# Performance work log

Hardware: AMD Instinct MI355X
Metric: run time of the kernel (lower is better)

Reference implementation:

```python
import jax, jax.numpy as jnp
import numpy as np

EPS = 1e-5

def spmm(rows, cols, vals, x, n_out):
    # COO sparse [n_out, n_in] @ x [n_in, d] -> [n_out, d]
    return jax.ops.segment_sum(vals[:, None] * x[cols], rows, num_segments=n_out)

def layernorm(x, g, b):
    mu = jnp.mean(x, axis=-1, keepdims=True)
    var = jnp.var(x, axis=-1, keepdims=True)
    return (x - mu) * jax.lax.rsqrt(var + EPS) * g + b

def setup_inputs() -> dict:
    key = jax.random.key(0)
    ks = jax.random.split(key, 32)
    N, D = 100000, 512
    N0, N1, N2 = 131072, 32768, 8192
    E_s0, E_s1 = 262144, 65536
    E_f0, E_f1 = 1048576, 262144
    s = 1.0 / np.sqrt(D)
    inp = {
        'x': jax.random.normal(ks[0], (N, D), jnp.float32),
        'hist0': jax.random.normal(ks[1], (N, D), jnp.float32),
        'hist1': jax.random.normal(ks[2], (N, D), jnp.float32),
        'w0': jax.random.normal(ks[3], (D, D), jnp.float32) * s,
        'b0': jax.random.normal(ks[4], (D,), jnp.float32) * s,
        'g0': jnp.ones((D,), jnp.float32),
        'beta0': jnp.zeros((D,), jnp.float32),
        'w1': jax.random.normal(ks[5], (D, D), jnp.float32) * s,
        'b1': jax.random.normal(ks[6], (D,), jnp.float32) * s,
        'sadj0_vals': jax.random.uniform(ks[7], (E_s0,), jnp.float32),
        'sadj1_vals': jax.random.uniform(ks[8], (E_s1,), jnp.float32),
        'fadj0_vals': jax.random.uniform(ks[9], (E_f0,), jnp.float32),
        'fadj1_vals': jax.random.uniform(ks[10], (E_f1,), jnp.float32),
        'sid0': jax.random.randint(ks[11], (N0,), 0, N),
        'sid1': jax.random.randint(ks[12], (N1,), 0, N),
        'sid2': jax.random.randint(ks[13], (N2,), 0, N),
        'fid0': jax.random.randint(ks[14], (N0,), 0, N),
        'fid1': jax.random.randint(ks[15], (N1,), 0, N),
        'sadj0_rows': jax.random.randint(ks[16], (E_s0,), 0, N1),
        'sadj0_cols': jax.random.randint(ks[17], (E_s0,), 0, N0),
        'sadj1_rows': jax.random.randint(ks[18], (E_s1,), 0, N2),
        'sadj1_cols': jax.random.randint(ks[19], (E_s1,), 0, N1),
        'fadj0_rows': jax.random.randint(ks[20], (E_f0,), 0, N1),
        'fadj0_cols': jax.random.randint(ks[21], (E_f0,), 0, N0),
        'fadj1_rows': jax.random.randint(ks[22], (E_f1,), 0, N2),
        'fadj1_cols': jax.random.randint(ks[23], (E_f1,), 0, N1),
    }
    return inp

def reference(x, hist0, hist1, w0, b0, g0, beta0, w1, b1,
              sadj0_vals, sadj1_vals, fadj0_vals, fadj1_vals,
              sid0, sid1, sid2, fid0, fid1,
              sadj0_rows, sadj0_cols, sadj1_rows, sadj1_cols,
              fadj0_rows, fadj0_cols, fadj1_rows, fadj1_cols):
    N1 = sid1.shape[0]
    N2 = sid2.shape[0]
    sg = jax.lax.stop_gradient
    # layer 0
    h = x[sid0]                                   # [N0, D]
    h = h - sg(hist0[sid0])                        # variance-reduction correction
    full = sg(spmm(fadj0_rows, fadj0_cols, fadj0_vals, hist0[fid0], N1))
    h = spmm(sadj0_rows, sadj0_cols, sadj0_vals, h, N1) + full  # [N1, D]
    h = h @ w0.T + b0
    h = jax.nn.relu(layernorm(h, g0, beta0))
    # layer 1 (last: no norm/relu)
    h = h - sg(hist1[sid1])
    full = sg(spmm(fadj1_rows, fadj1_cols, fadj1_vals, hist1[fid1], N2))
    h = spmm(sadj1_rows, sadj1_cols, sadj1_vals, h, N2) + full  # [N2, D]
    h = h @ w1.T + b1
    return jax.nn.log_softmax(h, axis=-1)
```

## Files before the change

kernel.cpp:

```cpp
#include <hip/hip_runtime.h>

#define D 512
#define NTAB 100000

typedef __bf16 bf16x8 __attribute__((ext_vector_type(8)));
typedef float f32x4 __attribute__((ext_vector_type(4)));
typedef float f32x2 __attribute__((ext_vector_type(2)));

__device__ __forceinline__ unsigned f2bf(float f){
  union { float f; unsigned u; } v; v.f = f;
  unsigned r = v.u + 0x7fffu + ((v.u >> 16) & 1u);
  return r >> 16;
}
__device__ __forceinline__ float bf2f(unsigned h){
  union { unsigned u; float f; } v; v.u = h << 16; return v.f;
}
__device__ __forceinline__ uint2 enc_fp8x8(f32x4 v0, f32x4 v1){
  int lo = __builtin_amdgcn_cvt_pk_fp8_f32(v0[0], v0[1], 0, false);
  lo     = __builtin_amdgcn_cvt_pk_fp8_f32(v0[2], v0[3], lo, true);
  int hi = __builtin_amdgcn_cvt_pk_fp8_f32(v1[0], v1[1], 0, false);
  hi     = __builtin_amdgcn_cvt_pk_fp8_f32(v1[2], v1[3], hi, true);
  return make_uint2((unsigned)lo, (unsigned)hi);
}

#define PER8 (NTAB*D/8)

#define MA_NS   6400
#define MA_GRID (MA_NS*5 + 512)

__global__ __launch_bounds__(256) void k_megaA(
    const int* __restrict__ s0r, int nS0,
    const int* __restrict__ f0r, int nF0, int* __restrict__ cnt0,
    const int* __restrict__ s1r, int nS1, int* __restrict__ cnt_s1,
    const int* __restrict__ f1r, int nF1, int* __restrict__ cnt_f1,
    const float* __restrict__ x, const float* __restrict__ hist0,
    unsigned char* __restrict__ TD,
    const float* __restrict__ w0, const float* __restrict__ w1,
    unsigned short* __restrict__ w0b, unsigned short* __restrict__ w1b)
{
  int b = blockIdx.x, t = threadIdx.x;
  if (b < MA_NS*5){
    int sb = b / 5, r = b % 5;
    if (r == 0){
      int i = sb*256 + t;
      if (i < nS0){ atomicAdd(&cnt0[s0r[i]], 1); return; }
      i -= nS0;
      if (i < nF0){ atomicAdd(&cnt0[f0r[i]], 1); return; }
      i -= nF0;
      if (i < nS1){ atomicAdd(&cnt_s1[s1r[i]], 1); return; }
      i -= nS1;
      atomicAdd(&cnt_f1[f1r[i]], 1);
      return;
    }
    {
      int ci = (sb*4 + (r-1))*256 + t;
      if (ci >= PER8) return;
      const f32x4* px = (const f32x4*)(x     + (size_t)ci*8);
      const f32x4* ph = (const f32x4*)(hist0 + (size_t)ci*8);
      f32x4 x0 = __builtin_nontemporal_load(px);
      f32x4 x1 = __builtin_nontemporal_load(px+1);
      f32x4 h0 = __builtin_nontemporal_load(ph);
      f32x4 h1 = __builtin_nontemporal_load(ph+1);
      *(uint2*)(TD + (size_t)ci*8)                    = enc_fp8x8(x0 - h0, x1 - h1);
      *(uint2*)(TD + (size_t)NTAB*D + (size_t)ci*8)   = enc_fp8x8(h0, h1);
      return;
    }
  } else {
    int i = (b - MA_NS*5)*256 + t;
    const float* src = (i < 65536) ? w0 : w1;
    unsigned short* dst = (i < 65536) ? w0b : w1b;
    int ii = (i < 65536) ? i : i - 65536;
    f32x4 v = *(const f32x4*)(src + (size_t)ii*4);
    ushort4 o;
    o.x = (unsigned short)f2bf(v[0]); o.y = (unsigned short)f2bf(v[1]);
    o.z = (unsigned short)f2bf(v[2]); o.w = (unsigned short)f2bf(v[3]);
    *(ushort4*)(dst + (size_t)ii*4) = o;
  }
}

__global__ __launch_bounds__(1024) void k_exscan3(
    const int* c0, int* r0, int n0,
    const int* c1, int* r1, int n1,
    const int* c2, int* r2, int n2)
{
  __shared__ int part[1024];
  const int* cnt; int* rp; int n;
  switch (blockIdx.x){
    case 0: cnt=c0; rp=r0; n=n0; break;
    case 1: cnt=c1; rp=r1; n=n1; break;
    default: cnt=c2; rp=r2; n=n2; break;
  }
  int t = threadIdx.x;
  int chunk = n >> 10;
  int base = t*chunk;
  int s = 0;
  for (int i=0;i<chunk;i++) s += cnt[base+i];
  part[t] = s; __syncthreads();
  for (int off=1; off<1024; off<<=1){
    int v = (t>=off) ? part[t-off] : 0;
    __syncthreads();
    part[t] += v;
    __syncthreads();
  }
  int run = (t==0) ? 0 : part[t-1];
  for (int i=0;i<chunk;i++){ rp[base+i] = run; run += cnt[base+i]; }
  if (t == 1023) rp[n] = run;
}

__global__ __launch_bounds__(256) void k_fill(
    const int* __restrict__ s0r, const int* __restrict__ s0c, const float* __restrict__ s0v, int nS0,
    const int* __restrict__ f0r, const int* __restrict__ f0c, const float* __restrict__ f0v, int nF0,
    const int* __restrict__ sid0, const int* __restrict__ fid0,
    const int* __restrict__ rp0, int* __restrict__ fill0, int2* __restrict__ bce0,
    const int* __restrict__ s1r, const int* __restrict__ s1c, const float* __restrict__ s1v, int nS1,
    const int* __restrict__ rp_s1, int* __restrict__ fill_s1, int2* __restrict__ bce_s1,
    const int* __restrict__ f1r, const int* __restrict__ f1c, const float* __restrict__ f1v,
    const int* __restrict__ fid1,
    const int* __restrict__ rp_f1, int* __restrict__ fill_f1, int2* __restrict__ bce_f1)
{
  int i = blockIdx.x*256 + threadIdx.x;
  if (i < nS0){
    int rr = s0r[i];
    int c  = sid0[s0c[i]];
    int p = atomicAdd(&fill0[rr], 1);
    bce0[rp0[rr] + p] = make_int2(c, __float_as_int(s0v[i]));
    return;
  }
  i -= nS0;
  if (i < nF0){
    int rr = f0r[i];
    int c  = NTAB + fid0[f0c[i]];
    int p = atomicAdd(&fill0[rr], 1);
    bce0[rp0[rr] + p] = make_int2(c, __float_as_int(f0v[i]));
    return;
  }
  i -= nF0;
  if (i < nS1){
    int rr = s1r[i];
    int p = atomicAdd(&fill_s1[rr], 1);
    bce_s1[rp_s1[rr] + p] = make_int2(s1c[i], __float_as_int(s1v[i]));
    return;
  }
  i -= nS1;
  {
    int rr = f1r[i];
    int c  = fid1[f1c[i]];
    int p = atomicAdd(&fill_f1[rr], 1);
    bce_f1[rp_f1[rr] + p] = make_int2(c, __float_as_int(f1v[i]));
  }
}

__device__ __forceinline__ void acc_bf16(float* a, uint4 p, float v){
  a[0] += v*bf2f(p.x & 0xffffu); a[1] += v*bf2f(p.x >> 16);
  a[2] += v*bf2f(p.y & 0xffffu); a[3] += v*bf2f(p.y >> 16);
  a[4] += v*bf2f(p.z & 0xffffu); a[5] += v*bf2f(p.z >> 16);
  a[6] += v*bf2f(p.w & 0xffffu); a[7] += v*bf2f(p.w >> 16);
}
__device__ __forceinline__ void acc_fp8(float* a, uint2 q, float v){
  f32x2 d0 = __builtin_amdgcn_cvt_pk_f32_fp8(q.x, false);
  f32x2 d1 = __builtin_amdgcn_cvt_pk_f32_fp8(q.x, true);
  f32x2 d2 = __builtin_amdgcn_cvt_pk_f32_fp8(q.y, false);
  f32x2 d3 = __builtin_amdgcn_cvt_pk_f32_fp8(q.y, true);
  a[0] += v*d0[0]; a[1] += v*d0[1]; a[2] += v*d1[0]; a[3] += v*d1[1];
  a[4] += v*d2[0]; a[5] += v*d2[1]; a[6] += v*d3[0]; a[7] += v*d3[1];
}

__device__ __forceinline__ void spmm_phase(
    const int* __restrict__ rp, const int2* __restrict__ be,
    const unsigned short* __restrict__ H, int row, int lane, float* a)
{
  int j = rp[row], je = rp[row+1];
  for (; j + 8 <= je; j += 8){
    int2 e[8]; uint4 p[8];
    #pragma unroll
    for (int u=0;u<8;u++) e[u] = be[j+u];
    #pragma unroll
    for (int u=0;u<8;u++) p[u] = *(const uint4*)(H + (size_t)e[u].x*D + lane*8);
    #pragma unroll
    for (int u=0;u<8;u++) acc_bf16(a, p[u], __int_as_float(e[u].y));
  }
  if (j + 4 <= je){
    int2 e[4]; uint4 p[4];
    #pragma unroll
    for (int u=0;u<4;u++) e[u] = be[j+u];
    #pragma unroll
    for (int u=0;u<4;u++) p[u] = *(const uint4*)(H + (size_t)e[u].x*D + lane*8);
    #pragma unroll
    for (int u=0;u<4;u++) acc_bf16(a, p[u], __int_as_float(e[u].y));
    j += 4;
  }
  for (; j < je; j++){
    int2 e = be[j];
    uint4 p = *(const uint4*)(H + (size_t)e.x*D + lane*8);
    acc_bf16(a, p, __int_as_float(e.y));
  }
}

__device__ __forceinline__ void spmm_phase_q8(
    const int* __restrict__ rp, const int2* __restrict__ be,
    const unsigned char* __restrict__ Q, int row, int lane, float* a)
{
  int j = rp[row], je = rp[row+1];
  for (; j + 8 <= je; j += 8){
    int2 e[8]; uint2 q[8];
    #pragma unroll
    for (int u=0;u<8;u++) e[u] = be[j+u];
    #pragma unroll
    for (int u=0;u<8;u++) q[u] = *(const uint2*)(Q + (size_t)e[u].x*D + lane*8);
    #pragma unroll
    for (int u=0;u<8;u++) acc_fp8(a, q[u], __int_as_float(e[u].y));
  }
  if (j + 4 <= je){
    int2 e[4]; uint2 q[4];
    #pragma unroll
    for (int u=0;u<4;u++) e[u] = be[j+u];
    #pragma unroll
    for (int u=0;u<4;u++) q[u] = *(const uint2*)(Q + (size_t)e[u].x*D + lane*8);
    #pragma unroll
    for (int u=0;u<4;u++) acc_fp8(a, q[u], __int_as_float(e[u].y));
    j += 4;
  }
  for (; j < je; j++){
    int2 e = be[j];
    uint2 q = *(const uint2*)(Q + (size_t)e.x*D + lane*8);
    acc_fp8(a, q, __int_as_float(e.y));
  }
}

__device__ __forceinline__ void store_row(unsigned short* out, int row, int lane, const float* a){
  uint4 o;
  o.x = f2bf(a[0]) | (f2bf(a[1]) << 16);
  o.y = f2bf(a[2]) | (f2bf(a[3]) << 16);
  o.z = f2bf(a[4]) | (f2bf(a[5]) << 16);
  o.w = f2bf(a[6]) | (f2bf(a[7]) << 16);
  *(uint4*)(out + (size_t)row*D + lane*8) = o;
}

#define SX_NS   1639
#define SX_GRID (SX_NS*7)
#define CONV_BLKS 3125

__global__ __launch_bounds__(256) void k_spmmX(
    const int* __restrict__ rp, const int2* __restrict__ be,
    const unsigned char* __restrict__ TD,
    unsigned short* __restrict__ out, int nrows,
    const float* __restrict__ hist1, unsigned short* __restrict__ H1b)
{
  int b = blockIdx.x, t = threadIdx.x;
  int sb = b / 7, r = b % 7;
  if (r < 5){
    int wid = t >> 6, lane = t & 63;
    int row = (sb*5 + r)*4 + wid;
    if (row >= nrows) return;
    float a[8] = {0.f,0.f,0.f,0.f,0.f,0.f,0.f,0.f};
    spmm_phase_q8(rp, be, TD, row, lane, a);
    store_row(out, row, lane, a);
  } else {
    int cb = sb*2 + (r-5);
    if (cb >= CONV_BLKS) return;
    #pragma unroll
    for (int k=0; k<8; k++){
      int ci = cb*256 + t + k*(CONV_BLKS*256);
      const f32x4* p = (const f32x4*)(hist1 + (size_t)ci*8);
      f32x4 v0 = __builtin_nontemporal_load(p);
      f32x4 v1 = __builtin_nontemporal_load(p+1);
      uint4 o;
      o.x = f2bf(v0[0]) | (f2bf(v0[1])<<16);
      o.y = f2bf(v0[2]) | (f2bf(v0[3])<<16);
      o.z = f2bf(v1[0]) | (f2bf(v1[1])<<16);
      o.w = f2bf(v1[2]) | (f2bf(v1[3])<<16);
      *(uint4*)(H1b + (size_t)ci*8) = o;
    }
  }
}

__global__ __launch_bounds__(256) void k_spmm_acc(
    const int* __restrict__ rp, const int2* __restrict__ be, const unsigned short* __restrict__ H,
    unsigned short* __restrict__ out, int nrows)
{
  int wid = threadIdx.x >> 6, lane = threadIdx.x & 63;
  int row = blockIdx.x*4 + wid;
  if (row >= nrows) return;
  float a[8];
  uint4 p = *(const uint4*)(out + (size_t)row*D + lane*8);
  a[0]=bf2f(p.x&0xffffu); a[1]=bf2f(p.x>>16); a[2]=bf2f(p.y&0xffffu); a[3]=bf2f(p.y>>16);
  a[4]=bf2f(p.z&0xffffu); a[5]=bf2f(p.z>>16); a[6]=bf2f(p.w&0xffffu); a[7]=bf2f(p.w>>16);
  spmm_phase(rp, be, H, row, lane, a);
  store_row(out, row, lane, a);
}

__device__ __forceinline__ void gload16(const unsigned short* g, unsigned short* l){
  __builtin_amdgcn_global_load_lds(
      (const __attribute__((address_space(1))) unsigned int*)(const void*)g,
      (__attribute__((address_space(3))) unsigned int*)(void*)l,
      16, 0, 0);
}

template<bool OUT_BF16>
__device__ __forceinline__ void gemm_block(
    const unsigned short* __restrict__ A,
    const unsigned short* __restrict__ B,
    const float* __restrict__ bias,
    void* __restrict__ Cv,
    int gemm_bid, unsigned short* Al, unsigned short* Bl)
{
  int bx = gemm_bid & 3, by = gemm_bid >> 2;
  int m0 = by << 7, n0 = bx << 7;
  int t = threadIdx.x, wave = t >> 6, lane = t & 63;
  int wr = wave >> 1, wc = wave & 1;
  f32x4 acc[4][4] = {};
  int flat = t << 3;
  int r0 = flat >> 5, cc = flat & 31;
  const unsigned short* pa = A + (size_t)(m0 + r0)*D + cc;
  const unsigned short* pb = B + (size_t)(n0 + r0)*D + cc;
  for (int k0 = 0; k0 < D; k0 += 32){
    gload16(pa + k0,                 &Al[flat]);
    gload16(pa + (size_t)64*D + k0,  &Al[flat + 2048]);
    gload16(pb + k0,                 &Bl[flat]);
    gload16(pb + (size_t)64*D + k0,  &Bl[flat + 2048]);
    __syncthreads();
    int arow = (wr << 6) | (lane & 15);
    int brow = (wc << 6) | (lane & 15);
    int kg   = (lane >> 4) << 3;
    bf16x8 af[4], bfr[4];
    #pragma unroll
    for (int mi=0; mi<4; mi++) af[mi]  = *(const bf16x8*)&Al[(arow + (mi<<4))*32 + kg];
    #pragma unroll
    for (int ni=0; ni<4; ni++) bfr[ni] = *(const bf16x8*)&Bl[(brow + (ni<<4))*32 + kg];
    #pragma unroll
    for (int mi=0; mi<4; mi++)
      #pragma unroll
      for (int ni=0; ni<4; ni++)
        acc[mi][ni] = __builtin_amdgcn_mfma_f32_16x16x32_bf16(af[mi], bfr[ni], acc[mi][ni], 0, 0, 0);
    __syncthreads();
  }
  int crow = m0 + (wr << 6) + ((lane >> 4) << 2);
  int ccol = n0 + (wc << 6) + (lane & 15);
  #pragma unroll
  for (int mi=0; mi<4; mi++){
    #pragma unroll
    for (int q=0; q<4; q++){
      int row = crow + (mi << 4) + q;
      #pragma unroll
      for (int ni=0; ni<4; ni++){
        float val = acc[mi][ni][q] + bias[ccol + (ni << 4)];
        if (OUT_BF16)
          ((unsigned short*)Cv)[(size_t)row*D + ccol + (ni << 4)] = (unsigned short)f2bf(val);
        else
          ((float*)Cv)[(size_t)row*D + ccol + (ni << 4)] = val;
      }
    }
  }
}

__global__ __launch_bounds__(256) void k_megaC(
    const unsigned short* __restrict__ A, const unsigned short* __restrict__ B,
    const float* __restrict__ bias, unsigned short* __restrict__ y1,
    const int* __restrict__ rpf, const int2* __restrict__ bef,
    const unsigned short* __restrict__ H1b, unsigned short* __restrict__ out2, int n2rows)
{
  __shared__ unsigned short Al[128*32];
  __shared__ unsigned short Bl[128*32];
  int b = blockIdx.x, t = threadIdx.x;
  int sb = b / 3, r = b % 3;
  if (r == 0){
    gemm_block<true>(A, B, bias, (void*)y1, sb, Al, Bl);
  } else {
    int wid = t >> 6, lane = t & 63;
    int row = (sb*2 + (r-1))*4 + wid;
    if (row >= n2rows) return;
    float a[8] = {0.f,0.f,0.f,0.f,0.f,0.f,0.f,0.f};
    spmm_phase(rpf, bef, H1b, row, lane, a);
    store_row(out2, row, lane, a);
  }
}

template<bool OUT_BF16>
__global__ __launch_bounds__(256) void k_gemm_bias(
    const unsigned short* __restrict__ A,
    const unsigned short* __restrict__ B,
    const float* __restrict__ bias,
    void* __restrict__ Cv,
    int M)
{
  __shared__ unsigned short Al[128*32];
  __shared__ unsigned short Bl[128*32];
  gemm_block<OUT_BF16>(A, B, bias, Cv, blockIdx.x, Al, Bl);
}

__global__ __launch_bounds__(256) void k_ln_relu_sub(
    const unsigned short* __restrict__ y, const float* __restrict__ gam, const float* __restrict__ bet,
    const unsigned short* __restrict__ H1b, const int* __restrict__ sid1,
    unsigned short* __restrict__ out)
{
  __shared__ float sh[8];
  int row = blockIdx.x, t = threadIdx.x;
  int c = t << 1;
  unsigned pv = *(const unsigned*)(y + (size_t)row*D + c);
  float vx = bf2f(pv & 0xffffu), vy = bf2f(pv >> 16);
  float s = vx + vy, ss = vx*vx + vy*vy;
  #pragma unroll
  for (int m=1; m<64; m<<=1){ s += __shfl_xor(s, m); ss += __shfl_xor(ss, m); }
  int wave = t >> 6, lane = t & 63;
  if (lane == 0){ sh[wave] = s; sh[4+wave] = ss; }
  __syncthreads();
  s  = sh[0]+sh[1]+sh[2]+sh[3];
  ss = sh[4]+sh[5]+sh[6]+sh[7];
  float mu  = s * (1.f/D);
  float var = ss * (1.f/D) - mu*mu;
  float rr  = rsqrtf(var + 1e-5f);
  int srow = sid1[row];
  unsigned hv = *(const unsigned*)(H1b + (size_t)srow*D + c);
  float o0 = fmaxf((vx - mu)*rr*gam[c]   + bet[c],   0.f) - bf2f(hv & 0xffffu);
  float o1 = fmaxf((vy - mu)*rr*gam[c+1] + bet[c+1], 0.f) - bf2f(hv >> 16);
  *(unsigned*)(out + (size_t)row*D + c) = f2bf(o0) | (f2bf(o1) << 16);
}

__global__ __launch_bounds__(256) void k_logsoftmax(const float* __restrict__ y, float* __restrict__ out){
  __shared__ float sh[8];
  int row = blockIdx.x, t = threadIdx.x;
  int c = t << 1;
  float2 v = *(const float2*)(y + (size_t)row*D + c);
  float m = fmaxf(v.x, v.y);
  #pragma unroll
  for (int k=1; k<64; k<<=1) m = fmaxf(m, __shfl_xor(m, k));
  int wave = t >> 6, lane = t & 63;
  if (lane == 0) sh[wave] = m;
  __syncthreads();
  m = fmaxf(fmaxf(sh[0], sh[1]), fmaxf(sh[2], sh[3]));
  __syncthreads();
  float e = expf(v.x - m) + expf(v.y - m);
  #pragma unroll
  for (int k=1; k<64; k<<=1) e += __shfl_xor(e, k);
  if (lane == 0) sh[4+wave] = e;
  __syncthreads();
  e = sh[4]+sh[5]+sh[6]+sh[7];
  float lse = m + logf(e);
  float2 o; o.x = v.x - lse; o.y = v.y - lse;
  *(float2*)(out + (size_t)row*D + c) = o;
}

extern "C" void kernel_launch(void* const* d_in, const int* in_sizes, int n_in,
                              void* d_out, int out_size, void* d_ws, size_t ws_size,
                              hipStream_t stream)
{
  const float* x     = (const float*)d_in[0];
  const float* hist0 = (const float*)d_in[1];
  const float* hist1 = (const float*)d_in[2];
  const float* w0    = (const float*)d_in[3];
  const float* b0    = (const float*)d_in[4];
  const float* g0    = (const float*)d_in[5];
  const float* beta0 = (const float*)d_in[6];
  const float* w1    = (const float*)d_in[7];
  const float* b1    = (const float*)d_in[8];
  const float* s0v   = (const float*)d_in[9];
  const float* s1v   = (const float*)d_in[10];
  const float* f0v   = (const float*)d_in[11];
  const float* f1v   = (const float*)d_in[12];
  const int* sid0    = (const int*)d_in[13];
  const int* sid1    = (const int*)d_in[14];
  const int* fid0    = (const int*)d_in[16];
  const int* fid1    = (const int*)d_in[17];
  const int* s0r     = (const int*)d_in[18];
  const int* s0c     = (const int*)d_in[19];
  const int* s1r     = (const int*)d_in[20];
  const int* s1c     = (const int*)d_in[21];
  const int* f0r     = (const int*)d_in[22];
  const int* f0c     = (const int*)d_in[23];
  const int* f1r     = (const int*)d_in[24];
  const int* f1c     = (const int*)d_in[25];

  const int N1 = 32768, N2 = 8192;
  const int Es0 = 262144, Es1 = 65536, Ef0 = 1048576, Ef1 = 262144;
  const int E0 = Es0 + Ef0;

  char* ws = (char*)d_ws;
  size_t off = 0;
  auto alloc = [&](size_t bytes)->char*{
    char* p = ws + off; off += (bytes + 255) & ~(size_t)255; return p;
  };
  char* TD_raw = alloc((size_t)2*NTAB*D);
  unsigned short* H1b = (unsigned short*)alloc((size_t)NTAB*D*2);
  unsigned short* h1   = (unsigned short*)alloc((size_t)N1*D*2);
  unsigned short* out1 = (unsigned short*)alloc((size_t)N1*D*2);
  unsigned short* w0b  = (unsigned short*)alloc((size_t)D*D*2);
  unsigned short* w1b  = (unsigned short*)alloc((size_t)D*D*2);
  int* meta = (int*)alloc((size_t)(2*N1 + 4*N2)*4);
  int* cnt0   = meta;            int* fill0   = cnt0 + N1;
  int* cnt_s1 = fill0 + N1;      int* fill_s1 = cnt_s1 + N2;
  int* cnt_f1 = fill_s1 + N2;    int* fill_f1 = cnt_f1 + N2;
  size_t metaBytes = (size_t)(2*N1 + 4*N2)*4;
  int* rp0   = (int*)alloc((size_t)(N1+1)*4);
  int* rp_s1 = (int*)alloc((size_t)(N2+1)*4);
  int* rp_f1 = (int*)alloc((size_t)(N2+1)*4);
  int2* bce0   = (int2*)alloc((size_t)E0*8);
  int2* bce_s1 = (int2*)alloc((size_t)Es1*8);
  int2* bce_f1 = (int2*)alloc((size_t)Ef1*8);

  unsigned char*  TD   = (unsigned char*)TD_raw;
  unsigned short* y1   = (unsigned short*)TD_raw;
  float*          y2   = (float*)(TD_raw + ((size_t)34<<20));
  unsigned short* out2 = (unsigned short*)(TD_raw + ((size_t)52<<20));
  float*          outp = (float*)d_out;

  hipMemsetAsync(meta, 0, metaBytes, stream);
  k_megaA<<<MA_GRID, 256, 0, stream>>>(
      s0r, Es0, f0r, Ef0, cnt0, s1r, Es1, cnt_s1, f1r, Ef1, cnt_f1,
      x, hist0, TD, w0, w1, w0b, w1b);
  k_exscan3<<<3, 1024, 0, stream>>>(cnt0, rp0, N1, cnt_s1, rp_s1, N2, cnt_f1, rp_f1, N2);
  k_fill<<<6400, 256, 0, stream>>>(
      s0r, s0c, s0v, Es0, f0r, f0c, f0v, Ef0, sid0, fid0, rp0, fill0, bce0,
      s1r, s1c, s1v, Es1, rp_s1, fill_s1, bce_s1,
      f1r, f1c, f1v, fid1, rp_f1, fill_f1, bce_f1);
  k_spmmX<<<SX_GRID, 256, 0, stream>>>(rp0, bce0, TD, out1, N1, hist1, H1b);
  k_megaC<<<1024*3, 256, 0, stream>>>(out1, w0b, b0, y1, rp_f1, bce_f1, H1b, out2, N2);
  k_ln_relu_sub<<<N1, 256, 0, stream>>>(y1, g0, beta0, H1b, sid1, h1);
  k_spmm_acc<<<N2/4, 256, 0, stream>>>(rp_s1, bce_s1, h1, out2, N2);
  k_gemm_bias<false><<<(N2/128)*4, 256, 0, stream>>>(out2, w1b, b1, (void*)y2, N2);
  k_logsoftmax<<<N2, 256, 0, stream>>>(y2, outp);
}
```

Measured before the change: 520.5 us.

## Quantize hist1 table to fp8 and move layer-1 CSR fill into spmmX

The full converted copy of hist1 is now stored as fp8 instead of bf16, which halves the conversion write traffic and the gather bytes in the layer-1 full-adjacency spmm (now done with the fp8 path). The layer-1 edge bucketing work moves out of the fill kernel into spare blocks of the spmmX kernel, overlapping it with the layer-0 spmm. The layer-norm subtraction now reads fp32 hist1 directly rather than the bf16 copy. The cost is fp8 precision error in the layer-1 full-neighbour aggregate.

New measurement: 543.2 us. +4.4%, slower.

```diff
diff --git a/kernel.cpp b/kernel.cpp
--- a/kernel.cpp
+++ b/kernel.cpp
@@ -107,16 +107,11 @@
   if (t == 1023) rp[n] = run;
 }
 
-__global__ __launch_bounds__(256) void k_fill(
+__global__ __launch_bounds__(256) void k_fill0(
     const int* __restrict__ s0r, const int* __restrict__ s0c, const float* __restrict__ s0v, int nS0,
     const int* __restrict__ f0r, const int* __restrict__ f0c, const float* __restrict__ f0v, int nF0,
     const int* __restrict__ sid0, const int* __restrict__ fid0,
-    const int* __restrict__ rp0, int* __restrict__ fill0, int2* __restrict__ bce0,
-    const int* __restrict__ s1r, const int* __restrict__ s1c, const float* __restrict__ s1v, int nS1,
-    const int* __restrict__ rp_s1, int* __restrict__ fill_s1, int2* __restrict__ bce_s1,
-    const int* __restrict__ f1r, const int* __restrict__ f1c, const float* __restrict__ f1v,
-    const int* __restrict__ fid1,
-    const int* __restrict__ rp_f1, int* __restrict__ fill_f1, int2* __restrict__ bce_f1)
+    const int* __restrict__ rp0, int* __restrict__ fill0, int2* __restrict__ bce0)
 {
   int i = blockIdx.x*256 + threadIdx.x;
   if (i < nS0){
@@ -127,26 +122,11 @@
     return;
   }
   i -= nS0;
-  if (i < nF0){
+  {
     int rr = f0r[i];
     int c  = NTAB + fid0[f0c[i]];
     int p = atomicAdd(&fill0[rr], 1);
     bce0[rp0[rr] + p] = make_int2(c, __float_as_int(f0v[i]));
-    return;
-  }
-  i -= nF0;
-  if (i < nS1){
-    int rr = s1r[i];
-    int p = atomicAdd(&fill_s1[rr], 1);
-    bce_s1[rp_s1[rr] + p] = make_int2(s1c[i], __float_as_int(s1v[i]));
-    return;
-  }
-  i -= nS1;
-  {
-    int rr = f1r[i];
-    int c  = fid1[f1c[i]];
-    int p = atomicAdd(&fill_f1[rr], 1);
-    bce_f1[rp_f1[rr] + p] = make_int2(c, __float_as_int(f1v[i]));
   }
 }
 
@@ -237,17 +217,22 @@
 }
 
 #define SX_NS   1639
-#define SX_GRID (SX_NS*7)
+#define SX_GRID (SX_NS*8)
 #define CONV_BLKS 3125
 
 __global__ __launch_bounds__(256) void k_spmmX(
     const int* __restrict__ rp, const int2* __restrict__ be,
     const unsigned char* __restrict__ TD,
     unsigned short* __restrict__ out, int nrows,
-    const float* __restrict__ hist1, unsigned short* __restrict__ H1b)
+    const float* __restrict__ hist1, unsigned char* __restrict__ H1q,
+    const int* __restrict__ s1r, const int* __restrict__ s1c, const float* __restrict__ s1v, int nS1,
+    const int* __restrict__ rp_s1, int* __restrict__ fill_s1, int2* __restrict__ bce_s1,
+    const int* __restrict__ f1r, const int* __restrict__ f1c, const float* __restrict__ f1v,
+    const int* __restrict__ fid1,
+    const int* __restrict__ rp_f1, int* __restrict__ fill_f1, int2* __restrict__ bce_f1)
 {
   int b = blockIdx.x, t = threadIdx.x;
-  int sb = b / 7, r = b % 7;
+  int sb = b / 8, r = b % 8;
   if (r < 5){
     int wid = t >> 6, lane = t & 63;
     int row = (sb*5 + r)*4 + wid;
@@ -255,7 +240,7 @@
     float a[8] = {0.f,0.f,0.f,0.f,0.f,0.f,0.f,0.f};
     spmm_phase_q8(rp, be, TD, row, lane, a);
     store_row(out, row, lane, a);
-  } else {
+  } else if (r < 7){
     int cb = sb*2 + (r-5);
     if (cb >= CONV_BLKS) return;
     #pragma unroll
@@ -264,12 +249,22 @@
       const f32x4* p = (const f32x4*)(hist1 + (size_t)ci*8);
       f32x4 v0 = __builtin_nontemporal_load(p);
       f32x4 v1 = __builtin_nontemporal_load(p+1);
-      uint4 o;
-      o.x = f2bf(v0[0]) | (f2bf(v0[1])<<16);
-      o.y = f2bf(v0[2]) | (f2bf(v0[3])<<16);
-      o.z = f2bf(v1[0]) | (f2bf(v1[1])<<16);
-      o.w = f2bf(v1[2]) | (f2bf(v1[3])<<16);
-      *(uint4*)(H1b + (size_t)ci*8) = o;
+      *(uint2*)(H1q + (size_t)ci*8) = enc_fp8x8(v0, v1);
+    }
+  } else {
+    int fb = sb;
+    if (fb >= 1280) return;
+    int i = fb*256 + t;
+    if (i < nS1){
+      int rr = s1r[i];
+      int p = atomicAdd(&fill_s1[rr], 1);
+      bce_s1[rp_s1[rr] + p] = make_int2(s1c[i], __float_as_int(s1v[i]));
+    } else {
+      i -= nS1;
+      int rr = f1r[i];
+      int c  = fid1[f1c[i]];
+      int p = atomicAdd(&fill_f1[rr], 1);
+      bce_f1[rp_f1[rr] + p] = make_int2(c, __float_as_int(f1v[i]));
     }
   }
 }
@@ -357,7 +352,7 @@
     const unsigned short* __restrict__ A, const unsigned short* __restrict__ B,
     const float* __restrict__ bias, unsigned short* __restrict__ y1,
     const int* __restrict__ rpf, const int2* __restrict__ bef,
-    const unsigned short* __restrict__ H1b, unsigned short* __restrict__ out2, int n2rows)
+    const unsigned char* __restrict__ H1q, unsigned short* __restrict__ out2, int n2rows)
 {
   __shared__ unsigned short Al[128*32];
   __shared__ unsigned short Bl[128*32];
@@ -370,7 +365,7 @@
     int row = (sb*2 + (r-1))*4 + wid;
     if (row >= n2rows) return;
     float a[8] = {0.f,0.f,0.f,0.f,0.f,0.f,0.f,0.f};
-    spmm_phase(rpf, bef, H1b, row, lane, a);
+    spmm_phase_q8(rpf, bef, H1q, row, lane, a);
     store_row(out2, row, lane, a);
   }
 }
@@ -390,7 +385,7 @@
 
 __global__ __launch_bounds__(256) void k_ln_relu_sub(
     const unsigned short* __restrict__ y, const float* __restrict__ gam, const float* __restrict__ bet,
-    const unsigned short* __restrict__ H1b, const int* __restrict__ sid1,
+    const float* __restrict__ hist1, const int* __restrict__ sid1,
     unsigned short* __restrict__ out)
 {
   __shared__ float sh[8];
@@ -410,9 +405,9 @@
   float var = ss * (1.f/D) - mu*mu;
   float rr  = rsqrtf(var + 1e-5f);
   int srow = sid1[row];
-  unsigned hv = *(const unsigned*)(H1b + (size_t)srow*D + c);
-  float o0 = fmaxf((vx - mu)*rr*gam[c]   + bet[c],   0.f) - bf2f(hv & 0xffffu);
-  float o1 = fmaxf((vy - mu)*rr*gam[c+1] + bet[c+1], 0.f) - bf2f(hv >> 16);
+  float2 hv = *(const float2*)(hist1 + (size_t)srow*D + c);
+  float o0 = fmaxf((vx - mu)*rr*gam[c]   + bet[c],   0.f) - hv.x;
+  float o1 = fmaxf((vy - mu)*rr*gam[c+1] + bet[c+1], 0.f) - hv.y;
   *(unsigned*)(out + (size_t)row*D + c) = f2bf(o0) | (f2bf(o1) << 16);
 }
 
@@ -480,14 +475,14 @@
     char* p = ws + off; off += (bytes + 255) & ~(size_t)255; return p;
   };
   char* TD_raw = alloc((size_t)2*NTAB*D);
-  unsigned short* H1b = (unsigned short*)alloc((size_t)NTAB*D*2);
+  unsigned char* H1q = (unsigned char*)alloc((size_t)NTAB*D);
   unsigned short* h1   = (unsigned short*)alloc((size_t)N1*D*2);
   unsigned short* out1 = (unsigned short*)alloc((size_t)N1*D*2);
   unsigned short* w0b  = (unsigned short*)alloc((size_t)D*D*2);
   unsigned short* w1b  = (unsigned short*)alloc((size_t)D*D*2);
   int* meta = (int*)alloc((size_t)(2*N1 + 4*N2)*4);
-  int* cnt0   = meta;            int* fill0   = cnt0 + N1;
-  int* cnt_s1 = fill0 + N1;      int* fill_s1 = cnt_s1 + N2;
+  int* cnt0   = meta;            int* fil0    = cnt0 + N1;
+  int* cnt_s1 = fil0 + N1;       int* fill_s1 = cnt_s1 + N2;
   int* cnt_f1 = fill_s1 + N2;    int* fill_f1 = cnt_f1 + N2;
   size_t metaBytes = (size_t)(2*N1 + 4*N2)*4;
   int* rp0   = (int*)alloc((size_t)(N1+1)*4);
@@ -508,13 +503,14 @@
       s0r, Es0, f0r, Ef0, cnt0, s1r, Es1, cnt_s1, f1r, Ef1, cnt_f1,
       x, hist0, TD, w0, w1, w0b, w1b);
   k_exscan3<<<3, 1024, 0, stream>>>(cnt0, rp0, N1, cnt_s1, rp_s1, N2, cnt_f1, rp_f1, N2);
-  k_fill<<<6400, 256, 0, stream>>>(
-      s0r, s0c, s0v, Es0, f0r, f0c, f0v, Ef0, sid0, fid0, rp0, fill0, bce0,
+  k_fill0<<<E0/256, 256, 0, stream>>>(
+      s0r, s0c, s0v, Es0, f0r, f0c, f0v, Ef0, sid0, fid0, rp0, fil0, bce0);
+  k_spmmX<<<SX_GRID, 256, 0, stream>>>(
+      rp0, bce0, TD, out1, N1, hist1, H1q,
       s1r, s1c, s1v, Es1, rp_s1, fill_s1, bce_s1,
       f1r, f1c, f1v, fid1, rp_f1, fill_f1, bce_f1);
-  k_spmmX<<<SX_GRID, 256, 0, stream>>>(rp0, bce0, TD, out1, N1, hist1, H1b);
-  k_megaC<<<1024*3, 256, 0, stream>>>(out1, w0b, b0, y1, rp_f1, bce_f1, H1b, out2, N2);
-  k_ln_relu_sub<<<N1, 256, 0, stream>>>(y1, g0, beta0, H1b, sid1, h1);
+  k_megaC<<<1024*3, 256, 0, stream>>>(out1, w0b, b0, y1, rp_f1, bce_f1, H1q, out2, N2);
+  k_ln_relu_sub<<<N1, 256, 0, stream>>>(y1, g0, beta0, hist1, sid1, h1);
   k_spmm_acc<<<N2/4, 256, 0, stream>>>(rp_s1, bce_s1, h1, out2, N2);
   k_gemm_bias<false><<<(N2/128)*4, 256, 0, stream>>>(out2, w1b, b1, (void*)y2, N2);
   k_logsoftmax<<<N2, 256, 0, stream>>>(y2, outp);
```
